# Performance work log

Hardware: AMD Instinct MI355X
Metric: run time of the kernel (lower is better)

## Reference

```python
import jax, jax.numpy as jnp
import numpy as np

N_NODES = 100000
N_EDGES = 1600000
IN_C, HID_C, OUT_C = 512, 128, 40


def gcn_conv(x, edge_index):
    """Symmetric-normalized sparse aggregation: out[d] = sum_e 1/sqrt(deg[s]*deg[d]) * x[s]."""
    n = x.shape[0]
    src, dst = edge_index[0], edge_index[1]
    deg = jax.ops.segment_sum(jnp.ones_like(dst, dtype=x.dtype), dst, num_segments=n)
    deg = jnp.maximum(deg, 1.0)  # guard isolated nodes
    dinv = jax.lax.rsqrt(deg)
    w = dinv[src] * dinv[dst]                      # [E]
    msg = x[src] * w[:, None]                      # [E, C] gather + scale
    return jax.ops.segment_sum(msg, dst, num_segments=n)  # scatter-add -> [N, C]


def setup_inputs() -> dict:
    key = jax.random.key(0)
    k1, k2, k3, k4 = jax.random.split(key, 4)
    x = jax.random.normal(k1, (N_NODES, IN_C), dtype=jnp.float32)
    edge_index = jax.random.randint(k2, (2, N_EDGES), 0, N_NODES, dtype=jnp.int64)
    # xavier_uniform with gain=1.414 (as in reset_parameters), zero biases
    def xavier(k, shape, gain=1.414):
        fan_out, fan_in = shape
        bound = gain * np.sqrt(6.0 / (fan_in + fan_out))
        return jax.random.uniform(k, shape, jnp.float32, -bound, bound)
    W0 = xavier(k3, (HID_C, IN_C))
    b0 = jnp.zeros((HID_C,), jnp.float32)
    W1 = xavier(k4, (OUT_C, HID_C))
    b1 = jnp.zeros((OUT_C,), jnp.float32)
    return {"x": x, "edge_index": edge_index, "W0": W0, "b0": b0, "W1": W1, "b1": b1}


def reference(x, edge_index, W0, b0, W1, b1):
    # layer 0: project -> sparse aggregate -> bias -> relu (dropout off in eval)
    h = x @ W0.T
    h = gcn_conv(h, edge_index)
    h = jax.nn.relu(h + b0)
    # final layer: project -> sparse aggregate -> bias (no activation)
    h = h @ W1.T
    h = gcn_conv(h, edge_index)
    return h + b1
```

## Files before the change

kernel.cpp:

```cpp
#include <hip/hip_runtime.h>
#include <hip/hip_bf16.h>
#include <cstddef>

#define N_NODES 100000
#define N_EDGES 1600000
#define IN_C 512
#define HID_C 128
#define OUT_C 40
#define OUT_CP 48
#define EPB 8000
#define NPART 200
#define NBKT 196
#define BSHIFT 9

typedef short bf16x8 __attribute__((ext_vector_type(8)));
typedef float f32x4 __attribute__((ext_vector_type(4)));

__device__ __forceinline__ float bf2f(unsigned short u) {
    union { unsigned int i; float f; } v; v.i = ((unsigned int)u) << 16; return v.f;
}
__device__ __forceinline__ float bf2f_lo(unsigned int u) {
    union { unsigned int i; float f; } v; v.i = u << 16; return v.f;
}
__device__ __forceinline__ float bf2f_hi(unsigned int u) {
    union { unsigned int i; float f; } v; v.i = u & 0xFFFF0000u; return v.f;
}
__device__ __forceinline__ unsigned short f2bf(float f) {
    union { float f; unsigned int i; } v; v.f = f;
    unsigned int x = v.i;
    return (unsigned short)((x + 0x7FFFu + ((x >> 16) & 1u)) >> 16);
}

__device__ __forceinline__ void glds16(const void* g, void* l) {
    __builtin_amdgcn_global_load_lds(
        (const __attribute__((address_space(1))) unsigned int*)g,
        (__attribute__((address_space(3))) unsigned int*)l,
        16, 0, 0);
}

__global__ void k_detect(const unsigned int* __restrict__ xbits,
                         const int* __restrict__ ei32, int* __restrict__ flags) {
    if (threadIdx.x == 0 && blockIdx.x == 0) {
        int inrange = 0;
        for (int i = 0; i < 64; i++) {
            unsigned int b = xbits[i * 33 + 1];
            int e = (int)((b >> 23) & 0xFFu);
            if (e >= 90 && e <= 160) inrange++;
        }
        flags[0] = (inrange >= 32) ? 0 : 1;
        int zeros = 0;
        for (int i = 0; i < 8; i++) if (ei32[2 * i + 1] == 0) zeros++;
        flags[1] = (zeros == 8) ? 1 : 0;
    }
}

__device__ __forceinline__ int load_src(const int* ei, int mi, int e) {
    return mi ? ei[2 * e] : ei[e];
}
__device__ __forceinline__ int load_dst(const int* ei, int mi, int e) {
    return mi ? ei[2 * (N_EDGES + e)] : ei[N_EDGES + e];
}

#define NW_TOTAL (IN_C * HID_C + HID_C * OUT_C + HID_C + OUT_C)
__global__ void k_norm_w(const void* __restrict__ W0, const void* __restrict__ W1,
                         const void* __restrict__ b0, const void* __restrict__ b1,
                         const int* __restrict__ flags,
                         unsigned short* __restrict__ w0n, unsigned short* __restrict__ w1n,
                         float* __restrict__ b0n, float* __restrict__ b1n) {
    int mf = flags[0];
    int i = blockIdx.x * 256 + threadIdx.x;
    if (i >= NW_TOTAL) return;
    if (i < IN_C * HID_C) {
        w0n[i] = mf ? ((const unsigned short*)W0)[i] : f2bf(((const float*)W0)[i]);
    } else if (i < IN_C * HID_C + HID_C * OUT_C) {
        int j = i - IN_C * HID_C;
        w1n[j] = mf ? ((const unsigned short*)W1)[j] : f2bf(((const float*)W1)[j]);
    } else if (i < IN_C * HID_C + HID_C * OUT_C + HID_C) {
        int j = i - IN_C * HID_C - HID_C * OUT_C;
        b0n[j] = mf ? bf2f(((const unsigned short*)b0)[j]) : ((const float*)b0)[j];
    } else {
        int j = i - IN_C * HID_C - HID_C * OUT_C - HID_C;
        b1n[j] = mf ? bf2f(((const unsigned short*)b1)[j]) : ((const float*)b1)[j];
    }
}

__global__ __launch_bounds__(256) void k_part1(const int* __restrict__ ei,
                                               const int* __restrict__ flags,
                                               int* __restrict__ bcnt,
                                               int* __restrict__ block_off) {
    __shared__ int h[NBKT];
    int t = threadIdx.x;
    for (int i = t; i < NBKT; i += 256) h[i] = 0;
    __syncthreads();
    int mi = flags[1];
    int base = blockIdx.x * EPB;
    for (int j = t; j < EPB; j += 256) {
        int e = base + j;
        if (e < N_EDGES) atomicAdd(&h[load_dst(ei, mi, e) >> BSHIFT], 1);
    }
    __syncthreads();
    for (int i = t; i < NBKT; i += 256)
        block_off[blockIdx.x * NBKT + i] = atomicAdd(&bcnt[i], h[i]);
}

__global__ void k_scan_bkt(const int* __restrict__ bcnt, int* __restrict__ bbase) {
    __shared__ int sm[256];
    int t = threadIdx.x;
    int v = (t < NBKT) ? bcnt[t] : 0;
    sm[t] = v; __syncthreads();
    for (int off = 1; off < 256; off <<= 1) {
        int a = (t >= off) ? sm[t - off] : 0;
        __syncthreads();
        sm[t] += a;
        __syncthreads();
    }
    if (t < NBKT) bbase[t] = sm[t] - v;
    if (t == NBKT - 1) bbase[NBKT] = sm[t];
}

__global__ __launch_bounds__(256) void k_part2(const int* __restrict__ ei,
                                               const int* __restrict__ flags,
                                               const int* __restrict__ bbase,
                                               const int* __restrict__ block_off,
                                               unsigned int* __restrict__ bedges) {
    __shared__ int cur[NBKT];
    int t = threadIdx.x;
    for (int i = t; i < NBKT; i += 256)
        cur[i] = bbase[i] + block_off[blockIdx.x * NBKT + i];
    __syncthreads();
    int mi = flags[1];
    int base = blockIdx.x * EPB;
    for (int j = t; j < EPB; j += 256) {
        int e = base + j;
        if (e < N_EDGES) {
            int d = load_dst(ei, mi, e);
            int s = load_src(ei, mi, e);
            int p = atomicAdd(&cur[d >> BSHIFT], 1);
            bedges[p] = ((unsigned int)s << BSHIFT) | (unsigned int)(d & 511);
        }
    }
}

__global__ __launch_bounds__(512) void k_bucket_csr(const unsigned int* __restrict__ bedges,
                                                    const int* __restrict__ bbase,
                                                    int* __restrict__ rowptr,
                                                    float* __restrict__ dinv,
                                                    int* __restrict__ col) {
    __shared__ int cnt[512];
    __shared__ int cur[512];
    int b = blockIdx.x, t = threadIdx.x;
    int ebeg = bbase[b], eend = bbase[b + 1];
    cnt[t] = 0;
    __syncthreads();
    for (int j = ebeg + t; j < eend; j += 512)
        atomicAdd(&cnt[bedges[j] & 511], 1);
    __syncthreads();
    int v = cnt[t];
    cur[t] = v; __syncthreads();
    for (int off = 1; off < 512; off <<= 1) {
        int a = (t >= off) ? cur[t - off] : 0;
        __syncthreads();
        cur[t] += a;
        __syncthreads();
    }
    int excl = cur[t] - v;
    int node = b * 512 + t;
    if (node < N_NODES) {
        rowptr[node] = ebeg + excl;
        float dd = (float)v; if (dd < 1.f) dd = 1.f;
        dinv[node] = rsqrtf(dd);
    } else if (node == N_NODES) {
        rowptr[N_NODES] = ebeg + excl;
    }
    __syncthreads();
    cur[t] = ebeg + excl;
    __syncthreads();
    for (int j = ebeg + t; j < eend; j += 512) {
        unsigned int pk = bedges[j];
        int p = atomicAdd(&cur[pk & 511], 1);
        col[p] = (int)(pk >> BSHIFT);
    }
}

#define G1_BUF 24576
#define G1_BOFF 16384

__device__ __forceinline__ void gemm1_f32_async(const float* __restrict__ xg,
                                                const unsigned short* __restrict__ w0n,
                                                const float* __restrict__ dinv,
                                                unsigned short* __restrict__ h1,
                                                char* __restrict__ smem,
                                                int node0, int t) {
    const int w = t >> 6;
    const int lane = t & 63;
    const int r16 = lane & 15;
    const int quad = lane >> 4;

    f32x4 acc[2][8];
#pragma unroll
    for (int m = 0; m < 2; m++)
#pragma unroll
        for (int c = 0; c < 8; c++) acc[m][c] = (f32x4){0.f, 0.f, 0.f, 0.f};

    const int lrow = lane >> 3;
    const int lch = (lane & 7) ^ lrow;
    const float* pa[4];
#pragma unroll
    for (int g = 0; g < 4; g++) {
        int r = node0 + w * 32 + 8 * g + lrow;
        if (r >= N_NODES) r = N_NODES - 1;
        pa[g] = xg + (size_t)r * IN_C + lch * 4;
    }
    const unsigned short* pb[2];
#pragma unroll
    for (int g = 0; g < 2; g++)
        pb[g] = w0n + (size_t)((2 * w + g) * 16 + r16) * IN_C + quad * 8;

    auto stage = [&](int buf, int ks) {
        char* Ab = smem + buf * G1_BUF + w * 4096;
        char* Bb = smem + buf * G1_BUF + G1_BOFF + w * 2048;
        glds16(pa[0] + ks, Ab);
        glds16(pa[1] + ks, Ab + 1024);
        glds16(pa[2] + ks, Ab + 2048);
        glds16(pa[3] + ks, Ab + 3072);
        glds16(pb[0] + ks, Bb);
        glds16(pb[1] + ks, Bb + 1024);
    };

    const int swz = r16 & 7;

    auto compute = [&](int buf) {
        const char* Ab = smem + buf * G1_BUF;
        const char* Bb = Ab + G1_BOFF;
        bf16x8 a[2];
#pragma unroll
        for (int m = 0; m < 2; m++) {
            int rowb = (w * 32 + m * 16 + r16) * 128;
            int c0 = ((2 * quad) ^ swz) * 16;
            int c1 = ((2 * quad + 1) ^ swz) * 16;
            float4 fa = *reinterpret_cast<const float4*>(Ab + rowb + c0);
            float4 fb = *reinterpret_cast<const float4*>(Ab + rowb + c1);
            a[m] = (bf16x8){(short)f2bf(fa.x), (short)f2bf(fa.y), (short)f2bf(fa.z), (short)f2bf(fa.w),
                            (short)f2bf(fb.x), (short)f2bf(fb.y), (short)f2bf(fb.z), (short)f2bf(fb.w)};
        }
#pragma unroll
        for (int ct = 0; ct < 8; ct++) {
            bf16x8 b = *reinterpret_cast<const bf16x8*>(Bb + ct * 1024 + lane * 16);
            acc[0][ct] = __builtin_amdgcn_mfma_f32_16x16x32_bf16(a[0], b, acc[0][ct], 0, 0, 0);
            acc[1][ct] = __builtin_amdgcn_mfma_f32_16x16x32_bf16(a[1], b, acc[1][ct], 0, 0, 0);
        }
    };

    stage(0, 0);
    stage(1, 32);
    for (int tt = 0; tt < 14; ++tt) {
        asm volatile("s_waitcnt vmcnt(6)" ::: "memory");
        __builtin_amdgcn_sched_barrier(0);
        __builtin_amdgcn_s_barrier();
        compute(tt & 1);
        __builtin_amdgcn_s_barrier();
        stage(tt & 1, (tt + 2) * 32);
    }
    asm volatile("s_waitcnt vmcnt(6)" ::: "memory");
    __builtin_amdgcn_sched_barrier(0);
    __builtin_amdgcn_s_barrier();
    compute(0);
    asm volatile("s_waitcnt vmcnt(0)" ::: "memory");
    __builtin_amdgcn_sched_barrier(0);
    __builtin_amdgcn_s_barrier();
    compute(1);

#pragma unroll
    for (int m = 0; m < 2; m++) {
#pragma unroll
        for (int r = 0; r < 4; r++) {
            int row = node0 + w * 32 + m * 16 + quad * 4 + r;
            if (row < N_NODES) {
                float dv = dinv[row];
#pragma unroll
                for (int ct = 0; ct < 8; ct++)
                    h1[(size_t)row * HID_C + ct * 16 + r16] = f2bf(acc[m][ct][r] * dv);
            }
        }
    }
}

__device__ __forceinline__ void gemm1_bf16_async(const unsigned short* __restrict__ xg,
                                                 const unsigned short* __restrict__ w0n,
                                                 const float* __restrict__ dinv,
                                                 unsigned short* __restrict__ h1,
                                                 unsigned short* __restrict__ smem,
                                                 int node0, int t) {
    const int w = t >> 6;
    const int lane = t & 63;
    const int r16 = lane & 15;
    const int quad = lane >> 4;

    f32x4 acc[2][8];
#pragma unroll
    for (int m = 0; m < 2; m++)
#pragma unroll
        for (int c = 0; c < 8; c++) acc[m][c] = (f32x4){0.f, 0.f, 0.f, 0.f};

    int rA0 = node0 + (2 * w) * 16 + r16;     if (rA0 >= N_NODES) rA0 = N_NODES - 1;
    int rA1 = node0 + (2 * w + 1) * 16 + r16; if (rA1 >= N_NODES) rA1 = N_NODES - 1;
    const unsigned short* pa0 = xg + (size_t)rA0 * IN_C + quad * 8;
    const unsigned short* pa1 = xg + (size_t)rA1 * IN_C + quad * 8;
    const unsigned short* pb0 = w0n + (size_t)((2 * w) * 16 + r16) * IN_C + quad * 8;
    const unsigned short* pb1 = w0n + (size_t)((2 * w + 1) * 16 + r16) * IN_C + quad * 8;

    auto stage = [&](int buf, int ks) {
        unsigned short* a = smem + buf * 8192 + (2 * w) * 512;
        glds16(pa0 + ks, a);
        glds16(pa1 + ks, a + 512);
        glds16(pb0 + ks, a + 4096);
        glds16(pb1 + ks, a + 4096 + 512);
    };

    const int fo = quad * 128 + r16 * 8;

    auto compute = [&](int buf) {
        const unsigned short* Ab = smem + buf * 8192;
        const unsigned short* Bb = Ab + 4096;
        bf16x8 a0 = *reinterpret_cast<const bf16x8*>(Ab + (2 * w) * 512 + fo);
        bf16x8 a1 = *reinterpret_cast<const bf16x8*>(Ab + (2 * w + 1) * 512 + fo);
#pragma unroll
        for (int ct = 0; ct < 8; ct++) {
            bf16x8 b = *reinterpret_cast<const bf16x8*>(Bb + ct * 512 + fo);
            acc[0][ct] = __builtin_amdgcn_mfma_f32_16x16x32_bf16(a0, b, acc[0][ct], 0, 0, 0);
            acc[1][ct] = __builtin_amdgcn_mfma_f32_16x16x32_bf16(a1, b, acc[1][ct], 0, 0, 0);
        }
    };

    stage(0, 0);
    __syncthreads();
    for (int tt = 0; tt < 15; ++tt) {
        int cur = tt & 1;
        stage(cur ^ 1, (tt + 1) * 32);
        compute(cur);
        __syncthreads();
    }
    compute(1);

#pragma unroll
    for (int m = 0; m < 2; m++) {
#pragma unroll
        for (int r = 0; r < 4; r++) {
            int row = node0 + w * 32 + m * 16 + quad * 4 + r;
            if (row < N_NODES) {
                float dv = dinv[row];
#pragma unroll
                for (int ct = 0; ct < 8; ct++)
                    h1[(size_t)row * HID_C + ct * 16 + r16] = f2bf(acc[m][ct][r] * dv);
            }
        }
    }
}

__global__ __launch_bounds__(256, 3) void k_gemm1(const void* __restrict__ x,
                                                  const unsigned short* __restrict__ w0n,
                                                  const int* __restrict__ flags,
                                                  const float* __restrict__ dinv,
                                                  unsigned short* __restrict__ h1) {
    __shared__ __align__(16) char smem[2 * G1_BUF];
    int node0 = blockIdx.x * 128;
    int t = threadIdx.x;
    if (flags[0]) gemm1_bf16_async((const unsigned short*)x, w0n, dinv, h1,
                                   (unsigned short*)smem, node0, t);
    else          gemm1_f32_async((const float*)x, w0n, dinv, h1, smem, node0, t);
}

__global__ __launch_bounds__(256) void k_agg1(const int* __restrict__ rowptr,
                                              const int* __restrict__ col,
                                              const float* __restrict__ dinv,
                                              const unsigned int* __restrict__ h1v,
                                              const float* __restrict__ b0n,
                                              unsigned int* __restrict__ h2v) {
    int w = threadIdx.x >> 6;
    int lane = threadIdx.x & 63;
    int d = blockIdx.x * 4 + w;
    if (d >= N_NODES) return;
    int beg = rowptr[d], end = rowptr[d + 1];
    float a0 = 0.f, a1 = 0.f;
    for (int j0 = beg; j0 < end; j0 += 16) {
        int s[16];
        unsigned int r[16];
        float m[16];
#pragma unroll
        for (int q = 0; q < 16; q++) {
            int jj = j0 + q;
            int jc = jj < end ? jj : end - 1;
            s[q] = col[jc];
            m[q] = jj < end ? 1.f : 0.f;
        }
#pragma unroll
        for (int q = 0; q < 16; q++) r[q] = h1v[(size_t)s[q] * 64 + lane];
#pragma unroll
        for (int q = 0; q < 16; q++) {
            a0 += m[q] * bf2f_lo(r[q]);
            a1 += m[q] * bf2f_hi(r[q]);
        }
    }
    float dv = dinv[d];
    float o0 = a0 * dv + b0n[2 * lane];
    float o1 = a1 * dv + b0n[2 * lane + 1];
    o0 = o0 > 0.f ? o0 : 0.f;
    o1 = o1 > 0.f ? o1 : 0.f;
    h2v[(size_t)d * 64 + lane] = (unsigned int)f2bf(o0) | ((unsigned int)f2bf(o1) << 16);
}

__global__ __launch_bounds__(256) void k_gemm2(const unsigned short* __restrict__ h2,
                                               const unsigned short* __restrict__ w1p,
                                               const float* __restrict__ dinv,
                                               float* __restrict__ p2) {
    int wave = (blockIdx.x * 256 + (int)threadIdx.x) >> 6;
    if (wave >= N_NODES / 16) return;
    int lane = threadIdx.x & 63;
    int r16 = lane & 15;
    int quad = lane >> 4;
    int node_base = wave * 16;

    f32x4 acc[3];
#pragma unroll
    for (int c = 0; c < 3; c++) acc[c] = (f32x4){0.f, 0.f, 0.f, 0.f};

    const unsigned short* arow = h2 + (size_t)(node_base + r16) * HID_C + quad * 8;
    const unsigned short* brow = w1p + (size_t)r16 * HID_C + quad * 8;

#pragma unroll
    for (int k0 = 0; k0 < HID_C; k0 += 32) {
        bf16x8 a = *reinterpret_cast<const bf16x8*>(arow + k0);
#pragma unroll
        for (int ct = 0; ct < 3; ct++) {
            bf16x8 b = *reinterpret_cast<const bf16x8*>(brow + (size_t)ct * 16 * HID_C + k0);
            acc[ct] = __builtin_amdgcn_mfma_f32_16x16x32_bf16(a, b, acc[ct], 0, 0, 0);
        }
    }

    float dv[4];
#pragma unroll
    for (int r = 0; r < 4; r++) dv[r] = dinv[node_base + quad * 4 + r];

#pragma unroll
    for (int ct = 0; ct < 3; ct++) {
        int chan = ct * 16 + r16;
        if (chan < OUT_C) {
#pragma unroll
            for (int r = 0; r < 4; r++) {
                p2[(size_t)(node_base + quad * 4 + r) * OUT_C + chan] = acc[ct][r] * dv[r];
            }
        }
    }
}

__global__ __launch_bounds__(256) void k_agg2(const int* __restrict__ rowptr,
                                              const int* __restrict__ col,
                                              const float* __restrict__ dinv,
                                              const float* __restrict__ p2,
                                              const float* __restrict__ b1n,
                                              const int* __restrict__ flags,
                                              void* __restrict__ out) {
    int w = threadIdx.x >> 6;
    int lane = threadIdx.x & 63;
    int d = blockIdx.x * 4 + w;
    if (d >= N_NODES || lane >= OUT_C) return;
    int beg = rowptr[d], end = rowptr[d + 1];
    float acc = 0.f;
    for (int j0 = beg; j0 < end; j0 += 16) {
        int s[16];
        float r[16];
        float m[16];
#pragma unroll
        for (int q = 0; q < 16; q++) {
            int jj = j0 + q;
            int jc = jj < end ? jj : end - 1;
            s[q] = col[jc];
            m[q] = jj < end ? 1.f : 0.f;
        }
#pragma unroll
        for (int q = 0; q < 16; q++) r[q] = p2[(size_t)s[q] * OUT_C + lane];
#pragma unroll
        for (int q = 0; q < 16; q++) acc += m[q] * r[q];
    }
    float v = acc * dinv[d] + b1n[lane];
    size_t idx = (size_t)d * OUT_C + lane;
    if (flags[0]) ((unsigned short*)out)[idx] = f2bf(v);
    else          ((float*)out)[idx] = v;
}

extern "C" void kernel_launch(void* const* d_in, const int* in_sizes, int n_in,
                              void* d_out, int out_size, void* d_ws, size_t ws_size,
                              hipStream_t stream) {
    const void* x  = d_in[0];
    const int* ei  = (const int*)d_in[1];
    const void* W0 = d_in[2];
    const void* b0 = d_in[3];
    const void* W1 = d_in[4];
    const void* b1 = d_in[5];

    char* ws = (char*)d_ws;
    size_t off = 0;
    auto alloc = [&](size_t bytes) {
        char* p = ws + off;
        off += (bytes + 511) & ~(size_t)511;
        return p;
    };
    int*   flags   = (int*)  alloc(sizeof(int) * 2);
    int*   rowptr  = (int*)  alloc(sizeof(int) * (N_NODES + 1));
    float* dinv    = (float*)alloc(sizeof(float) * N_NODES);
    int*   col     = (int*)  alloc(sizeof(int) * N_EDGES);
    int*   bcnt    = (int*)  alloc(sizeof(int) * NBKT);
    int*   bbase   = (int*)  alloc(sizeof(int) * (NBKT + 1));
    int*   bloff   = (int*)  alloc(sizeof(int) * NPART * NBKT);
    unsigned int* bedges = (unsigned int*)alloc(sizeof(unsigned int) * N_EDGES);
    unsigned short* w0n = (unsigned short*)alloc(sizeof(unsigned short) * IN_C * HID_C);
    unsigned short* w1n = (unsigned short*)alloc(sizeof(unsigned short) * OUT_CP * HID_C);
    float* b0n = (float*)alloc(sizeof(float) * HID_C);
    float* b1n = (float*)alloc(sizeof(float) * OUT_C);
    unsigned short* h1 = (unsigned short*)alloc(sizeof(unsigned short) * (size_t)N_NODES * HID_C);
    unsigned short* h2 = (unsigned short*)alloc(sizeof(unsigned short) * (size_t)N_NODES * HID_C);
    float* p2 = (float*)h1;

    k_detect<<<1, 64, 0, stream>>>((const unsigned int*)x, ei, flags);
    hipMemsetAsync(w1n, 0, sizeof(unsigned short) * OUT_CP * HID_C, stream);
    k_norm_w<<<(NW_TOTAL + 255) / 256, 256, 0, stream>>>(W0, W1, b0, b1, flags, w0n, w1n, b0n, b1n);

    hipMemsetAsync(bcnt, 0, sizeof(int) * NBKT, stream);
    k_part1<<<NPART, 256, 0, stream>>>(ei, flags, bcnt, bloff);
    k_scan_bkt<<<1, 256, 0, stream>>>(bcnt, bbase);
    k_part2<<<NPART, 256, 0, stream>>>(ei, flags, bbase, bloff, bedges);
    k_bucket_csr<<<NBKT, 512, 0, stream>>>(bedges, bbase, rowptr, dinv, col);

    k_gemm1<<<(N_NODES + 127) / 128, 256, 0, stream>>>(x, w0n, flags, dinv, h1);
    k_agg1<<<(N_NODES + 3) / 4, 256, 0, stream>>>(rowptr, col, dinv,
                                                  (const unsigned int*)h1, b0n,
                                                  (unsigned int*)h2);
    k_gemm2<<<(N_NODES / 16 + 3) / 4, 256, 0, stream>>>(h2, w1n, dinv, p2);
    k_agg2<<<(N_NODES + 3) / 4, 256, 0, stream>>>(rowptr, col, dinv, p2, b1n, flags, d_out);
}
```

Measured before the change: 525.9 us.

## Fuse layer-1 aggregation with second projection GEMM via shared-memory dot products

Result: slower. 552.7 us (+5.1%).

```diff
diff --git a/kernel.cpp b/kernel.cpp
--- a/kernel.cpp
+++ b/kernel.cpp
@@ -7,7 +7,6 @@
 #define IN_C 512
 #define HID_C 128
 #define OUT_C 40
-#define OUT_CP 48
 #define EPB 8000
 #define NPART 200
 #define NBKT 196
@@ -370,14 +369,25 @@
     else          gemm1_f32_async((const float*)x, w0n, dinv, h1, smem, node0, t);
 }
 
-__global__ __launch_bounds__(256) void k_agg1(const int* __restrict__ rowptr,
-                                              const int* __restrict__ col,
-                                              const float* __restrict__ dinv,
-                                              const unsigned int* __restrict__ h1v,
-                                              const float* __restrict__ b0n,
-                                              unsigned int* __restrict__ h2v) {
-    int w = threadIdx.x >> 6;
-    int lane = threadIdx.x & 63;
+#define W1PAD 132
+__global__ __launch_bounds__(256) void k_agg1g2(const int* __restrict__ rowptr,
+                                                const int* __restrict__ col,
+                                                const float* __restrict__ dinv,
+                                                const unsigned int* __restrict__ h1v,
+                                                const float* __restrict__ b0n,
+                                                const unsigned short* __restrict__ w1n,
+                                                float* __restrict__ p2) {
+    __shared__ float W1f[OUT_C][W1PAD];
+    __shared__ float hrow[4][HID_C];
+    int t = threadIdx.x;
+    for (int i = t; i < OUT_C * HID_C; i += 256) {
+        int c = i >> 7, k = i & 127;
+        W1f[c][k] = bf2f(w1n[i]);
+    }
+    __syncthreads();
+
+    int w = t >> 6;
+    int lane = t & 63;
     int d = blockIdx.x * 4 + w;
     if (d >= N_NODES) return;
     int beg = rowptr[d], end = rowptr[d + 1];
@@ -406,50 +416,19 @@
     float o1 = a1 * dv + b0n[2 * lane + 1];
     o0 = o0 > 0.f ? o0 : 0.f;
     o1 = o1 > 0.f ? o1 : 0.f;
-    h2v[(size_t)d * 64 + lane] = (unsigned int)f2bf(o0) | ((unsigned int)f2bf(o1) << 16);
-}
-
-__global__ __launch_bounds__(256) void k_gemm2(const unsigned short* __restrict__ h2,
-                                               const unsigned short* __restrict__ w1p,
-                                               const float* __restrict__ dinv,
-                                               float* __restrict__ p2) {
-    int wave = (blockIdx.x * 256 + (int)threadIdx.x) >> 6;
-    if (wave >= N_NODES / 16) return;
-    int lane = threadIdx.x & 63;
-    int r16 = lane & 15;
-    int quad = lane >> 4;
-    int node_base = wave * 16;
-
-    f32x4 acc[3];
-#pragma unroll
-    for (int c = 0; c < 3; c++) acc[c] = (f32x4){0.f, 0.f, 0.f, 0.f};
-
-    const unsigned short* arow = h2 + (size_t)(node_base + r16) * HID_C + quad * 8;
-    const unsigned short* brow = w1p + (size_t)r16 * HID_C + quad * 8;
-
-#pragma unroll
-    for (int k0 = 0; k0 < HID_C; k0 += 32) {
-        bf16x8 a = *reinterpret_cast<const bf16x8*>(arow + k0);
-#pragma unroll
-        for (int ct = 0; ct < 3; ct++) {
-            bf16x8 b = *reinterpret_cast<const bf16x8*>(brow + (size_t)ct * 16 * HID_C + k0);
-            acc[ct] = __builtin_amdgcn_mfma_f32_16x16x32_bf16(a, b, acc[ct], 0, 0, 0);
-        }
-    }
-
-    float dv[4];
-#pragma unroll
-    for (int r = 0; r < 4; r++) dv[r] = dinv[node_base + quad * 4 + r];
-
-#pragma unroll
-    for (int ct = 0; ct < 3; ct++) {
-        int chan = ct * 16 + r16;
-        if (chan < OUT_C) {
-#pragma unroll
-            for (int r = 0; r < 4; r++) {
-                p2[(size_t)(node_base + quad * 4 + r) * OUT_C + chan] = acc[ct][r] * dv[r];
-            }
-        }
+    *reinterpret_cast<float2*>(&hrow[w][2 * lane]) = (float2){o0, o1};
+    asm volatile("s_waitcnt lgkmcnt(0)" ::: "memory");
+    __builtin_amdgcn_sched_barrier(0);
+
+    if (lane < OUT_C) {
+        float accv = 0.f;
+#pragma unroll
+        for (int k0 = 0; k0 < HID_C; k0 += 4) {
+            float4 hv = *reinterpret_cast<const float4*>(&hrow[w][k0]);
+            float4 wv = *reinterpret_cast<const float4*>(&W1f[lane][k0]);
+            accv += hv.x * wv.x + hv.y * wv.y + hv.z * wv.z + hv.w * wv.w;
+        }
+        p2[(size_t)d * OUT_C + lane] = accv * dv;
     }
 }
 
@@ -514,15 +493,13 @@
     int*   bloff   = (int*)  alloc(sizeof(int) * NPART * NBKT);
     unsigned int* bedges = (unsigned int*)alloc(sizeof(unsigned int) * N_EDGES);
     unsigned short* w0n = (unsigned short*)alloc(sizeof(unsigned short) * IN_C * HID_C);
-    unsigned short* w1n = (unsigned short*)alloc(sizeof(unsigned short) * OUT_CP * HID_C);
+    unsigned short* w1n = (unsigned short*)alloc(sizeof(unsigned short) * HID_C * OUT_C);
     float* b0n = (float*)alloc(sizeof(float) * HID_C);
     float* b1n = (float*)alloc(sizeof(float) * OUT_C);
     unsigned short* h1 = (unsigned short*)alloc(sizeof(unsigned short) * (size_t)N_NODES * HID_C);
-    unsigned short* h2 = (unsigned short*)alloc(sizeof(unsigned short) * (size_t)N_NODES * HID_C);
-    float* p2 = (float*)h1;
+    float* p2 = (float*)alloc(sizeof(float) * (size_t)N_NODES * OUT_C);
 
     k_detect<<<1, 64, 0, stream>>>((const unsigned int*)x, ei, flags);
-    hipMemsetAsync(w1n, 0, sizeof(unsigned short) * OUT_CP * HID_C, stream);
     k_norm_w<<<(NW_TOTAL + 255) / 256, 256, 0, stream>>>(W0, W1, b0, b1, flags, w0n, w1n, b0n, b1n);
 
     hipMemsetAsync(bcnt, 0, sizeof(int) * NBKT, stream);
@@ -532,9 +509,8 @@
     k_bucket_csr<<<NBKT, 512, 0, stream>>>(bedges, bbase, rowptr, dinv, col);
 
     k_gemm1<<<(N_NODES + 127) / 128, 256, 0, stream>>>(x, w0n, flags, dinv, h1);
-    k_agg1<<<(N_NODES + 3) / 4, 256, 0, stream>>>(rowptr, col, dinv,
-                                                  (const unsigned int*)h1, b0n,
-                                                  (unsigned int*)h2);
-    k_gemm2<<<(N_NODES / 16 + 3) / 4, 256, 0, stream>>>(h2, w1n, dinv, p2);
+    k_agg1g2<<<(N_NODES + 3) / 4, 256, 0, stream>>>(rowptr, col, dinv,
+                                                    (const unsigned int*)h1, b0n,
+                                                    w1n, p2);
     k_agg2<<<(N_NODES + 3) / 4, 256, 0, stream>>>(rowptr, col, dinv, p2, b1n, flags, d_out);
 }
```
